# Kernel tuning notes

Measured on AMD Instinct MI355X. Metric: run time of the kernel, lower is better.

The kernel has to match this reference:

```python
import jax, jax.numpy as jnp
import numpy as np


def _rbf(x, z):
    # x: [..., M, D], z: [N, D] or [..., K, D] -> pairwise exp(-0.5*||x-z||^2)
    x2 = jnp.sum(x * x, axis=-1)[..., :, None]
    z2 = jnp.sum(z * z, axis=-1)[..., None, :]
    xz = jnp.einsum('...md,...nd->...mn', x, z)
    sq = jnp.maximum(x2 + z2 - 2.0 * xz, 0.0)
    return jnp.exp(-0.5 * sq)


def setup_inputs() -> dict:
    key = jax.random.key(0)
    k1, k2, k3, k4, k5 = jax.random.split(key, 5)
    B, M, P, N = 8, 1024, 256, 4096
    X = jax.random.normal(k1, (B, M, P), dtype=jnp.float32)
    A = jax.random.randint(k2, (B, M), 0, 2, dtype=jnp.int32)
    XA_train = jax.random.normal(k3, (N, P + 1), dtype=jnp.float32)
    alpha = jax.random.normal(k4, (N,), dtype=jnp.float32)
    K_inv = jax.random.normal(k5, (N, N), dtype=jnp.float32) * 0.01
    return {"X": X, "A": A, "XA_train": XA_train, "alpha": alpha, "K_inv": K_inv}


def reference(X, A, XA_train, alpha, K_inv):
    # XA = concat([X, A[..., None]])  -> [B, M, P+1]
    XA = jnp.concatenate([X, A.astype(X.dtype)[..., None]], axis=-1)
    # kernel(XA, XA_train): [B, M, N]
    Kxz = _rbf(XA, XA_train)
    # f_loc = einsum('...mn,...n->...m', K(XA, train), alpha)
    f_loc = jnp.einsum('bmn,n->bm', Kxz, alpha)
    # kernel(XA_train, XA) == Kxz^T for a symmetric kernel
    Kzx = jnp.swapaxes(Kxz, -1, -2)  # [B, N, M]
    # cov_train_x = K_inv @ K(train, XA): [B, N, M]
    cov_train_x = jnp.einsum('tn,bnk->btk', K_inv, Kzx)
    # f_cov = K(XA, XA) - K(XA, train) @ cov_train_x: [B, M, M]
    Kxx = _rbf(XA, XA)
    f_cov = Kxx - jnp.einsum('bmn,bnk->bmk', Kxz, cov_train_x)
    f_var = jnp.diagonal(f_cov, axis1=-2, axis2=-1)  # [B, M]
    return f_loc, f_var
```

## Files before the change

### kernel.cpp

```cpp
#include <hip/hip_runtime.h>
#include <math.h>

#define R_ROWS 8192
#define NP     4096
#define DREAL  257
#define DPAD   288

#define BM 128
#define BN 128
#define BK 32
#define LDSS 32
#define NBLKX (R_ROWS / BM)
#define NBLKY (NP / BN)

using frag8 = __attribute__((ext_vector_type(8))) short;
using f32x4 = __attribute__((ext_vector_type(4))) float;

static __device__ __forceinline__ float bf2f(unsigned short u) {
    return __uint_as_float(((unsigned int)u) << 16);
}
static __device__ __forceinline__ unsigned short f2bf(float f) {
    unsigned int u = __float_as_uint(f);
    unsigned int lsb = (u >> 16) & 1u;
    u += 0x7fffu + lsb;
    return (unsigned short)(u >> 16);
}

static __device__ __forceinline__ void gll16(const unsigned short* g, unsigned short* l) {
    __builtin_amdgcn_global_load_lds(
        (const __attribute__((address_space(1))) unsigned int*)g,
        (__attribute__((address_space(3))) unsigned int*)l, 16, 0, 0);
}

__global__ void prep_all(const float* __restrict__ X, const int* __restrict__ A,
                         const float* __restrict__ Z,
                         unsigned short* __restrict__ XAb, unsigned short* __restrict__ Zb,
                         float* __restrict__ x2, float* __restrict__ z2,
                         char* __restrict__ zreg,
                         float* __restrict__ out) {
    int b = blockIdx.x;
    int tid = threadIdx.x;
    uint4 zz = {0, 0, 0, 0};
    if (b < 11) {
        int off = b * 4096 + tid * 16;
        if (off < 41472) *(uint4*)(zreg + off) = zz;
    } else if (b < 19) {
        int off = (b - 11) * 4096 + tid * 16;
        *(uint4*)((char*)out + off) = zz;
    }

    int row  = b * 4 + (tid >> 6);
    int lane = tid & 63;
    float s = 0.f;
    if (row < R_ROWS) {
        const float* xr = X + (size_t)row * 256;
        unsigned short* o = XAb + (size_t)row * DPAD;
#pragma unroll
        for (int i = 0; i < 4; i++) {
            float v = xr[lane + 64 * i];
            s += v * v;
            o[lane + 64 * i] = f2bf(v);
        }
        if (lane == 0) {
            float a = (float)A[row];
            o[256] = f2bf(a);
            s += a * a;
        }
        if (lane >= 33) o[257 + (lane - 33)] = 0;
#pragma unroll
        for (int off = 32; off; off >>= 1) s += __shfl_down(s, off, 64);
        if (lane == 0) x2[row] = s;
    } else {
        int zr_i = row - R_ROWS;
        if (zr_i >= NP) return;
        const float* zr = Z + (size_t)zr_i * DREAL;
        unsigned short* o = Zb + (size_t)zr_i * DPAD;
#pragma unroll
        for (int i = 0; i < 4; i++) {
            float v = zr[lane + 64 * i];
            s += v * v;
            o[lane + 64 * i] = f2bf(v);
        }
        if (lane < 32) {
            int idx = 256 + lane;
            float v = (idx < DREAL) ? zr[idx] : 0.f;
            s += v * v;
            o[idx] = f2bf(v);
        }
#pragma unroll
        for (int off = 32; off; off >>= 1) s += __shfl_down(s, off, 64);
        if (lane == 0) z2[zr_i] = s;
    }
}

__global__ __launch_bounds__(256, 3) void gemm_kxz(
    const unsigned short* __restrict__ Abuf,
    const unsigned short* __restrict__ Bbuf,
    const float* __restrict__ x2, const float* __restrict__ z2,
    const float* __restrict__ alpha,
    unsigned short* __restrict__ Kb,
    float* __restrict__ floc_out,
    int* __restrict__ rowflag, int* __restrict__ tileflag)
{
    __shared__ unsigned short sA[3][BM * LDSS];
    __shared__ unsigned short sB[3][BN * LDSS];
    __shared__ int sAnyW[4];
    const int m0 = blockIdx.x * BM, n0 = blockIdx.y * BN;
    const int tid = threadIdx.x, lane = tid & 63, wave = tid >> 6;
    const int wr = wave >> 1, wc = wave & 1;
    const int q = lane >> 4, rr = lane & 15;
    const int grow = lane >> 2, gcol = (lane & 3) * 8;

    f32x4 acc[4][4] = {};
    for (int kk = 0; kk < DPAD; kk += 3 * BK) {
#pragma unroll
        for (int s3 = 0; s3 < 3; s3++) {
            int ks = kk + s3 * BK;
#pragma unroll
            for (int c = 0; c < 2; c++) {
                int r = wave * 32 + c * 16 + grow;
                unsigned short* la = &sA[s3][(wave * 32 + c * 16) * LDSS];
                unsigned short* lb = &sB[s3][(wave * 32 + c * 16) * LDSS];
                gll16(Abuf + (size_t)(m0 + r) * DPAD + ks + gcol, la);
                gll16(Bbuf + (size_t)(n0 + r) * DPAD + ks + gcol, lb);
            }
        }
        __syncthreads();
#pragma unroll
        for (int s3 = 0; s3 < 3; s3++) {
            frag8 af[4], bfr[4];
#pragma unroll
            for (int i = 0; i < 4; i++) {
                af[i]  = *(const frag8*)(&sA[s3][(wr * 64 + i * 16 + rr) * LDSS + q * 8]);
                bfr[i] = *(const frag8*)(&sB[s3][(wc * 64 + i * 16 + rr) * LDSS + q * 8]);
            }
#pragma unroll
            for (int i = 0; i < 4; i++)
#pragma unroll
                for (int j = 0; j < 4; j++)
                    acc[i][j] = __builtin_amdgcn_mfma_f32_16x16x32_bf16(af[i], bfr[j], acc[i][j], 0, 0, 0);
        }
        __syncthreads();
    }
    float zn[4];
#pragma unroll
    for (int j = 0; j < 4; j++) zn[j] = z2[n0 + wc * 64 + j * 16 + rr];
    bool anyl = false;
#pragma unroll
    for (int i = 0; i < 4; i++)
#pragma unroll
        for (int reg = 0; reg < 4; reg++) {
            float x = x2[m0 + wr * 64 + i * 16 + q * 4 + reg];
#pragma unroll
            for (int j = 0; j < 4; j++) {
                float d = x + zn[j] - 2.0f * acc[i][j][reg];
                anyl |= !(d >= 186.0f);
            }
        }
    unsigned long long wb = __ballot(anyl);
    if (lane == 0) sAnyW[wave] = (wb != 0ULL) ? 1 : 0;
    __syncthreads();
    if (sAnyW[0] | sAnyW[1] | sAnyW[2] | sAnyW[3]) {
        float av[4];
#pragma unroll
        for (int j = 0; j < 4; j++) av[j] = alpha[n0 + wc * 64 + j * 16 + rr];
        unsigned int wany = 0;
#pragma unroll
        for (int i = 0; i < 4; i++) {
#pragma unroll
            for (int reg = 0; reg < 4; reg++) {
                int ml = wr * 64 + i * 16 + q * 4 + reg;
                float x = x2[m0 + ml];
                float s = 0.f;
#pragma unroll
                for (int j = 0; j < 4; j++) {
                    float d = fmaxf(x + zn[j] - 2.0f * acc[i][j][reg], 0.0f);
                    unsigned short bv = f2bf(__expf(-0.5f * d));
                    wany |= bv;
                    Kb[(size_t)(m0 + ml) * NP + n0 + wc * 64 + j * 16 + rr] = bv;
                    s += bf2f(bv) * av[j];
                }
                s += __shfl_xor(s, 1, 64);
                s += __shfl_xor(s, 2, 64);
                s += __shfl_xor(s, 4, 64);
                s += __shfl_xor(s, 8, 64);
                if (rr == 0 && s != 0.0f) atomicAdd(&floc_out[m0 + ml], s);
            }
        }
        unsigned long long b2 = __ballot(wany != 0);
        if (lane == 0 && b2 != 0ULL) {
            atomicOr(&tileflag[blockIdx.x * NBLKY + blockIdx.y], 1);
            atomicOr(&rowflag[blockIdx.x], 1);
        }
    }
}

__global__ __launch_bounds__(256, 4) void gemm_q(
    const unsigned short* __restrict__ Kb,
    const float* __restrict__ Kinv,
    float* __restrict__ q_acc,
    const int* __restrict__ rowflag, const int* __restrict__ tileflag)
{
    const int m0 = blockIdx.x * BM, t0 = blockIdx.y * BN;
    if (rowflag[blockIdx.x] == 0) return;

    __shared__ unsigned short sA[BM * LDSS];
    __shared__ unsigned short sB[BN * LDSS];
    const int tid = threadIdx.x, lane = tid & 63, wave = tid >> 6;
    const int wr = wave >> 1, wc = wave & 1;
    const int q = lane >> 4, rr = lane & 15;
    const int grow = lane >> 2, gcol = (lane & 3) * 8;
    const int mblk = blockIdx.x * NBLKY;

    f32x4 acc[4][4] = {};
    for (int kb = 0; kb < NBLKY; kb++) {
        if (tileflag[mblk + kb] == 0) continue;
        int kk0 = kb * BN;
#pragma unroll
        for (int k2 = 0; k2 < BN; k2 += BK) {
            int kk = kk0 + k2;
#pragma unroll
            for (int c = 0; c < 2; c++) {
                int rl = wave * 32 + c * 16 + grow;
                gll16(Kb + (size_t)(m0 + rl) * NP + kk + gcol,
                      &sA[(wave * 32 + c * 16) * LDSS]);
                const float* gp = Kinv + (size_t)(t0 + rl) * NP + kk + gcol;
                float4 v0 = *(const float4*)gp;
                float4 v1 = *(const float4*)(gp + 4);
                unsigned short tmp[8];
                tmp[0] = f2bf(v0.x); tmp[1] = f2bf(v0.y);
                tmp[2] = f2bf(v0.z); tmp[3] = f2bf(v0.w);
                tmp[4] = f2bf(v1.x); tmp[5] = f2bf(v1.y);
                tmp[6] = f2bf(v1.z); tmp[7] = f2bf(v1.w);
                *(uint4*)(&sB[rl * LDSS + gcol]) = *(const uint4*)tmp;
            }
            __syncthreads();
            frag8 af[4], bfr[4];
#pragma unroll
            for (int i = 0; i < 4; i++) {
                af[i]  = *(const frag8*)(&sA[(wr * 64 + i * 16 + rr) * LDSS + q * 8]);
                bfr[i] = *(const frag8*)(&sB[(wc * 64 + i * 16 + rr) * LDSS + q * 8]);
            }
#pragma unroll
            for (int i = 0; i < 4; i++)
#pragma unroll
                for (int j = 0; j < 4; j++)
                    acc[i][j] = __builtin_amdgcn_mfma_f32_16x16x32_bf16(af[i], bfr[j], acc[i][j], 0, 0, 0);
            __syncthreads();
        }
    }
    if (tileflag[mblk + blockIdx.y] == 0) return;
#pragma unroll
    for (int i = 0; i < 4; i++) {
#pragma unroll
        for (int reg = 0; reg < 4; reg++) {
            int m = m0 + wr * 64 + i * 16 + q * 4 + reg;
            float s = 0.f;
#pragma unroll
            for (int j = 0; j < 4; j++) {
                int t = t0 + wc * 64 + j * 16 + rr;
                s += acc[i][j][reg] * bf2f(Kb[(size_t)m * NP + t]);
            }
            s += __shfl_xor(s, 1, 64);
            s += __shfl_xor(s, 2, 64);
            s += __shfl_xor(s, 4, 64);
            s += __shfl_xor(s, 8, 64);
            if (rr == 0 && s != 0.0f) atomicAdd(&q_acc[m], s);
        }
    }
}

__global__ void finalize(const float* __restrict__ q_acc, float* __restrict__ out) {
    int m = blockIdx.x * blockDim.x + threadIdx.x;
    if (m < R_ROWS) out[R_ROWS + m] = 1.0f - q_acc[m];
}

extern "C" void kernel_launch(void* const* d_in, const int* in_sizes, int n_in,
                              void* d_out, int out_size, void* d_ws, size_t ws_size,
                              hipStream_t stream) {
    const float* X     = (const float*)d_in[0];
    const int*   A     = (const int*)d_in[1];
    const float* Z     = (const float*)d_in[2];
    const float* alpha = (const float*)d_in[3];
    const float* Kinv  = (const float*)d_in[4];
    float* out = (float*)d_out;

    char* ws = (char*)d_ws;
    unsigned short* XAb = (unsigned short*)(ws);
    unsigned short* Zb  = (unsigned short*)(ws + 4718592);
    float* x2       = (float*)(ws + 7077888);
    float* z2       = (float*)(ws + 7110656);
    float*        q_acc    = (float*)(ws + 7127040);
    int*          rowflag  = (int*)  (ws + 7159808);
    int*          tileflag = (int*)  (ws + 7160064);
    unsigned short* Kb = (unsigned short*)(ws + 7168512);

    prep_all<<<(R_ROWS + NP) / 4, 256, 0, stream>>>(X, A, Z, XAb, Zb, x2, z2,
                                                    (char*)q_acc, out);
    gemm_kxz<<<dim3(NBLKX, NBLKY), 256, 0, stream>>>(XAb, Zb, x2, z2, alpha, Kb,
                                                     out, rowflag, tileflag);
    gemm_q<<<dim3(NBLKX, NBLKY), 256, 0, stream>>>(Kb, Kinv, q_acc, rowflag, tileflag);
    finalize<<<R_ROWS / 256, 256, 0, stream>>>(q_acc, out);
}
```

Measured before the change: 130.4 us.

## Drop K padding to 256 by handling the 257th feature as a rank-one epilogue term

Shrinks the inner dimension of the Kxz GEMM from a padded 288 to exactly 256 by pulling the 257th feature (the action column) out of the bf16 matrices. Its contribution a_m*z_n,256 is added in the epilogue with an FMA, which removes one of three K-phases of loads and MFMAs. The gemm_kxz pipeline becomes two phases of four K-slabs with launch bounds lowered to 2 waves per SIMD. The finalize kernel is also removed: the variance output is pre-set to 1 and gemm_q atomically subtracts into it. The trade-off is larger LDS use and lower occupancy in gemm_kxz, plus the last feature is now multiplied in fp32 rather than bf16.

```diff
diff --git a/kernel.cpp b/kernel.cpp
--- a/kernel.cpp
+++ b/kernel.cpp
@@ -4,7 +4,7 @@
 #define R_ROWS 8192
 #define NP     4096
 #define DREAL  257
-#define DPAD   288
+#define DPAD   256
 
 #define BM 128
 #define BN 128
@@ -36,17 +36,23 @@
                          const float* __restrict__ Z,
                          unsigned short* __restrict__ XAb, unsigned short* __restrict__ Zb,
                          float* __restrict__ x2, float* __restrict__ z2,
-                         char* __restrict__ zreg,
+                         float* __restrict__ zlast, float* __restrict__ af,
+                         char* __restrict__ flags,
                          float* __restrict__ out) {
     int b = blockIdx.x;
     int tid = threadIdx.x;
-    uint4 zz = {0, 0, 0, 0};
-    if (b < 11) {
+    if (b < 3) {
         int off = b * 4096 + tid * 16;
-        if (off < 41472) *(uint4*)(zreg + off) = zz;
+        uint4 zz = {0, 0, 0, 0};
+        if (off < 8448) *(uint4*)(flags + off) = zz;
+    } else if (b < 11) {
+        int off = (b - 3) * 1024 + tid * 4;
+        float4 zz4 = {0.f, 0.f, 0.f, 0.f};
+        *(float4*)(out + off) = zz4;
     } else if (b < 19) {
-        int off = (b - 11) * 4096 + tid * 16;
-        *(uint4*)((char*)out + off) = zz;
+        int off = R_ROWS + (b - 11) * 1024 + tid * 4;
+        float4 oo = {1.f, 1.f, 1.f, 1.f};
+        *(float4*)(out + off) = oo;
     }
 
     int row  = b * 4 + (tid >> 6);
@@ -54,7 +60,7 @@
     float s = 0.f;
     if (row < R_ROWS) {
         const float* xr = X + (size_t)row * 256;
-        unsigned short* o = XAb + (size_t)row * DPAD;
+        unsigned short* o = XAb + (size_t)row * 256;
 #pragma unroll
         for (int i = 0; i < 4; i++) {
             float v = xr[lane + 64 * i];
@@ -63,48 +69,45 @@
         }
         if (lane == 0) {
             float a = (float)A[row];
-            o[256] = f2bf(a);
+            af[row] = a;
             s += a * a;
         }
-        if (lane >= 33) o[257 + (lane - 33)] = 0;
 #pragma unroll
         for (int off = 32; off; off >>= 1) s += __shfl_down(s, off, 64);
         if (lane == 0) x2[row] = s;
     } else {
-        int zr_i = row - R_ROWS;
-        if (zr_i >= NP) return;
-        const float* zr = Z + (size_t)zr_i * DREAL;
-        unsigned short* o = Zb + (size_t)zr_i * DPAD;
+        int zi = row - R_ROWS;
+        if (zi >= NP) return;
+        const float* zr = Z + (size_t)zi * DREAL;
+        unsigned short* o = Zb + (size_t)zi * 256;
 #pragma unroll
         for (int i = 0; i < 4; i++) {
             float v = zr[lane + 64 * i];
             s += v * v;
             o[lane + 64 * i] = f2bf(v);
         }
-        if (lane < 32) {
-            int idx = 256 + lane;
-            float v = (idx < DREAL) ? zr[idx] : 0.f;
+        if (lane == 0) {
+            float v = zr[256];
             s += v * v;
-            o[idx] = f2bf(v);
+            zlast[zi] = bf2f(f2bf(v));
         }
 #pragma unroll
         for (int off = 32; off; off >>= 1) s += __shfl_down(s, off, 64);
-        if (lane == 0) z2[zr_i] = s;
-    }
-}
-
-__global__ __launch_bounds__(256, 3) void gemm_kxz(
+        if (lane == 0) z2[zi] = s;
+    }
+}
+
+__global__ __launch_bounds__(256, 2) void gemm_kxz(
     const unsigned short* __restrict__ Abuf,
     const unsigned short* __restrict__ Bbuf,
     const float* __restrict__ x2, const float* __restrict__ z2,
+    const float* __restrict__ zlast, const float* __restrict__ af,
     const float* __restrict__ alpha,
     unsigned short* __restrict__ Kb,
     float* __restrict__ floc_out,
     int* __restrict__ rowflag, int* __restrict__ tileflag)
 {
-    __shared__ unsigned short sA[3][BM * LDSS];
-    __shared__ unsigned short sB[3][BN * LDSS];
-    __shared__ int sAnyW[4];
+    __shared__ unsigned short sh[2][4][BM * LDSS];
     const int m0 = blockIdx.x * BM, n0 = blockIdx.y * BN;
     const int tid = threadIdx.x, lane = tid & 63, wave = tid >> 6;
     const int wr = wave >> 1, wc = wave & 1;
@@ -112,55 +115,65 @@
     const int grow = lane >> 2, gcol = (lane & 3) * 8;
 
     f32x4 acc[4][4] = {};
-    for (int kk = 0; kk < DPAD; kk += 3 * BK) {
-#pragma unroll
-        for (int s3 = 0; s3 < 3; s3++) {
-            int ks = kk + s3 * BK;
+#pragma unroll
+    for (int ph = 0; ph < 2; ph++) {
+        int k0 = ph * 128;
+#pragma unroll
+        for (int s3 = 0; s3 < 4; s3++) {
+            int ks = k0 + s3 * BK;
 #pragma unroll
             for (int c = 0; c < 2; c++) {
                 int r = wave * 32 + c * 16 + grow;
-                unsigned short* la = &sA[s3][(wave * 32 + c * 16) * LDSS];
-                unsigned short* lb = &sB[s3][(wave * 32 + c * 16) * LDSS];
-                gll16(Abuf + (size_t)(m0 + r) * DPAD + ks + gcol, la);
-                gll16(Bbuf + (size_t)(n0 + r) * DPAD + ks + gcol, lb);
+                gll16(Abuf + (size_t)(m0 + r) * 256 + ks + gcol,
+                      &sh[0][s3][(wave * 32 + c * 16) * LDSS]);
+                gll16(Bbuf + (size_t)(n0 + r) * 256 + ks + gcol,
+                      &sh[1][s3][(wave * 32 + c * 16) * LDSS]);
             }
         }
         __syncthreads();
 #pragma unroll
-        for (int s3 = 0; s3 < 3; s3++) {
-            frag8 af[4], bfr[4];
+        for (int s3 = 0; s3 < 4; s3++) {
+            frag8 afr[4], bfr[4];
 #pragma unroll
             for (int i = 0; i < 4; i++) {
-                af[i]  = *(const frag8*)(&sA[s3][(wr * 64 + i * 16 + rr) * LDSS + q * 8]);
-                bfr[i] = *(const frag8*)(&sB[s3][(wc * 64 + i * 16 + rr) * LDSS + q * 8]);
+                afr[i] = *(const frag8*)(&sh[0][s3][(wr * 64 + i * 16 + rr) * LDSS + q * 8]);
+                bfr[i] = *(const frag8*)(&sh[1][s3][(wc * 64 + i * 16 + rr) * LDSS + q * 8]);
             }
 #pragma unroll
             for (int i = 0; i < 4; i++)
 #pragma unroll
                 for (int j = 0; j < 4; j++)
-                    acc[i][j] = __builtin_amdgcn_mfma_f32_16x16x32_bf16(af[i], bfr[j], acc[i][j], 0, 0, 0);
+                    acc[i][j] = __builtin_amdgcn_mfma_f32_16x16x32_bf16(afr[i], bfr[j], acc[i][j], 0, 0, 0);
         }
         __syncthreads();
     }
-    float zn[4];
-#pragma unroll
-    for (int j = 0; j < 4; j++) zn[j] = z2[n0 + wc * 64 + j * 16 + rr];
+    float zn[4], zl[4];
+#pragma unroll
+    for (int j = 0; j < 4; j++) {
+        int n = n0 + wc * 64 + j * 16 + rr;
+        zn[j] = z2[n];
+        zl[j] = zlast[n];
+    }
     bool anyl = false;
 #pragma unroll
     for (int i = 0; i < 4; i++)
 #pragma unroll
         for (int reg = 0; reg < 4; reg++) {
-            float x = x2[m0 + wr * 64 + i * 16 + q * 4 + reg];
+            int ml = wr * 64 + i * 16 + q * 4 + reg;
+            float x  = x2[m0 + ml];
+            float am = af[m0 + ml];
 #pragma unroll
             for (int j = 0; j < 4; j++) {
-                float d = x + zn[j] - 2.0f * acc[i][j][reg];
+                float xz = fmaf(am, zl[j], acc[i][j][reg]);
+                float d = x + zn[j] - 2.0f * xz;
                 anyl |= !(d >= 186.0f);
             }
         }
     unsigned long long wb = __ballot(anyl);
-    if (lane == 0) sAnyW[wave] = (wb != 0ULL) ? 1 : 0;
+    int* sflag = (int*)&sh[0][0][0];
+    if (lane == 0) sflag[wave] = (wb != 0ULL) ? 1 : 0;
     __syncthreads();
-    if (sAnyW[0] | sAnyW[1] | sAnyW[2] | sAnyW[3]) {
+    if (sflag[0] | sflag[1] | sflag[2] | sflag[3]) {
         float av[4];
 #pragma unroll
         for (int j = 0; j < 4; j++) av[j] = alpha[n0 + wc * 64 + j * 16 + rr];
@@ -170,11 +183,13 @@
 #pragma unroll
             for (int reg = 0; reg < 4; reg++) {
                 int ml = wr * 64 + i * 16 + q * 4 + reg;
-                float x = x2[m0 + ml];
+                float x  = x2[m0 + ml];
+                float am = af[m0 + ml];
                 float s = 0.f;
 #pragma unroll
                 for (int j = 0; j < 4; j++) {
-                    float d = fmaxf(x + zn[j] - 2.0f * acc[i][j][reg], 0.0f);
+                    float xz = fmaf(am, zl[j], acc[i][j][reg]);
+                    float d = fmaxf(x + zn[j] - 2.0f * xz, 0.0f);
                     unsigned short bv = f2bf(__expf(-0.5f * d));
                     wany |= bv;
                     Kb[(size_t)(m0 + ml) * NP + n0 + wc * 64 + j * 16 + rr] = bv;
@@ -198,7 +213,7 @@
 __global__ __launch_bounds__(256, 4) void gemm_q(
     const unsigned short* __restrict__ Kb,
     const float* __restrict__ Kinv,
-    float* __restrict__ q_acc,
+    float* __restrict__ out,
     const int* __restrict__ rowflag, const int* __restrict__ tileflag)
 {
     const int m0 = blockIdx.x * BM, t0 = blockIdx.y * BN;
@@ -235,17 +250,17 @@
                 *(uint4*)(&sB[rl * LDSS + gcol]) = *(const uint4*)tmp;
             }
             __syncthreads();
-            frag8 af[4], bfr[4];
+            frag8 afr[4], bfr[4];
 #pragma unroll
             for (int i = 0; i < 4; i++) {
-                af[i]  = *(const frag8*)(&sA[(wr * 64 + i * 16 + rr) * LDSS + q * 8]);
+                afr[i] = *(const frag8*)(&sA[(wr * 64 + i * 16 + rr) * LDSS + q * 8]);
                 bfr[i] = *(const frag8*)(&sB[(wc * 64 + i * 16 + rr) * LDSS + q * 8]);
             }
 #pragma unroll
             for (int i = 0; i < 4; i++)
 #pragma unroll
                 for (int j = 0; j < 4; j++)
-                    acc[i][j] = __builtin_amdgcn_mfma_f32_16x16x32_bf16(af[i], bfr[j], acc[i][j], 0, 0, 0);
+                    acc[i][j] = __builtin_amdgcn_mfma_f32_16x16x32_bf16(afr[i], bfr[j], acc[i][j], 0, 0, 0);
             __syncthreads();
         }
     }
@@ -265,14 +280,9 @@
             s += __shfl_xor(s, 2, 64);
             s += __shfl_xor(s, 4, 64);
             s += __shfl_xor(s, 8, 64);
-            if (rr == 0 && s != 0.0f) atomicAdd(&q_acc[m], s);
-        }
-    }
-}
-
-__global__ void finalize(const float* __restrict__ q_acc, float* __restrict__ out) {
-    int m = blockIdx.x * blockDim.x + threadIdx.x;
-    if (m < R_ROWS) out[R_ROWS + m] = 1.0f - q_acc[m];
+            if (rr == 0 && s != 0.0f) atomicAdd(&out[R_ROWS + m], -s);
+        }
+    }
 }
 
 extern "C" void kernel_launch(void* const* d_in, const int* in_sizes, int n_in,
@@ -287,18 +297,18 @@
 
     char* ws = (char*)d_ws;
     unsigned short* XAb = (unsigned short*)(ws);
-    unsigned short* Zb  = (unsigned short*)(ws + 4718592);
-    float* x2       = (float*)(ws + 7077888);
-    float* z2       = (float*)(ws + 7110656);
-    float*        q_acc    = (float*)(ws + 7127040);
-    int*          rowflag  = (int*)  (ws + 7159808);
-    int*          tileflag = (int*)  (ws + 7160064);
-    unsigned short* Kb = (unsigned short*)(ws + 7168512);
-
-    prep_all<<<(R_ROWS + NP) / 4, 256, 0, stream>>>(X, A, Z, XAb, Zb, x2, z2,
-                                                    (char*)q_acc, out);
-    gemm_kxz<<<dim3(NBLKX, NBLKY), 256, 0, stream>>>(XAb, Zb, x2, z2, alpha, Kb,
-                                                     out, rowflag, tileflag);
-    gemm_q<<<dim3(NBLKX, NBLKY), 256, 0, stream>>>(Kb, Kinv, q_acc, rowflag, tileflag);
-    finalize<<<R_ROWS / 256, 256, 0, stream>>>(q_acc, out);
-}
+    unsigned short* Zb  = (unsigned short*)(ws + 4194304);
+    float* x2    = (float*)(ws + 6291456);
+    float* z2    = (float*)(ws + 6324224);
+    float* zlast = (float*)(ws + 6340608);
+    float* af    = (float*)(ws + 6356992);
+    int*   rowflag  = (int*)(ws + 6389760);
+    int*   tileflag = (int*)(ws + 6390016);
+    unsigned short* Kb = (unsigned short*)(ws + 6398208);
+
+    prep_all<<<(R_ROWS + NP) / 4, 256, 0, stream>>>(X, A, Z, XAb, Zb, x2, z2, zlast, af,
+                                                    (char*)rowflag, out);
+    gemm_kxz<<<dim3(NBLKX, NBLKY), 256, 0, stream>>>(XAb, Zb, x2, z2, zlast, af, alpha,
+                                                     Kb, out, rowflag, tileflag);
+    gemm_q<<<dim3(NBLKX, NBLKY), 256, 0, stream>>>(Kb, Kinv, out, rowflag, tileflag);
+}
```

Result: faster. 127.9 us (-2.0%).
